# Kernel optimization log

Measured on AMD Instinct MI355X. Metric: run time of the kernel, lower is better.

The kernel has to match this reference:

```python
import jax, jax.numpy as jnp
import numpy as np
from collections import deque

N, IN_DIM, H, B, L = 512, 64, 128, 256, 2
SOURCE = 105
E_UND = 2048


def _build_graph_and_masks():
    rng = np.random.default_rng(0)
    s = rng.integers(0, N, E_UND)
    d = rng.integers(0, N, E_UND)
    edge_index = np.stack([np.concatenate([s, d]), np.concatenate([d, s])]).astype(np.int32)
    # BFS depths from source (undirected)
    adj = [[] for _ in range(N)]
    for a, b in zip(edge_index[0], edge_index[1]):
        adj[int(a)].append(int(b))
    depths = np.full(N, np.inf)
    depths[SOURCE] = 0.0
    q = deque([SOURCE]); seen = {SOURCE}
    while q:
        u = q.popleft()
        for v in adj[u]:
            if v not in seen:
                seen.add(v); depths[v] = depths[u] + 1.0; q.append(v)
    finite = np.isfinite(depths)
    maxd = depths[finite].max() if finite.any() else 0.0
    depths[~finite] = maxd + 1.0
    adj_mask = np.zeros((N, N), np.float32)
    adj_mask[edge_index[0], edge_index[1]] = 1.0
    adj_mask[edge_index[1], edge_index[0]] = 1.0
    np.fill_diagonal(adj_mask, 1.0)
    direction_mask = (depths[None, :] <= depths[:, None]).astype(np.float32)
    # admittance_matrix is None -> uniform init, then masked
    initial_causal = (np.ones((N, N), np.float32) / N) * adj_mask * direction_mask
    return edge_index, adj_mask, direction_mask, initial_causal


def setup_inputs() -> dict:
    key = jax.random.key(0)
    ks = jax.random.split(key, 16)
    edge_index, adj_mask, direction_mask, initial_causal = _build_graph_and_masks()
    w = lambda k, shp: jax.random.normal(k, shp, jnp.float32) * 0.02
    return {
        'x': jax.random.normal(ks[0], (B, N, IN_DIM), jnp.float32),
        'edge_index': jnp.asarray(edge_index),
        'adj_mask': jnp.asarray(adj_mask),
        'direction_mask': jnp.asarray(direction_mask),
        'causal_logits': jnp.asarray(initial_causal),  # nn.Parameter init
        'W_in': w(ks[1], (IN_DIM, H)), 'b_in': jnp.zeros((H,), jnp.float32),
        'Wq': w(ks[2], (H, H)), 'bq': jnp.zeros((H,), jnp.float32),
        'Wk': w(ks[3], (H, H)), 'bk': jnp.zeros((H,), jnp.float32),
        'Wv': w(ks[4], (H, H)), 'bv': jnp.zeros((H,), jnp.float32),
        'gcn_W': w(ks[5], (L, H, H)), 'gcn_b': jnp.zeros((L, H), jnp.float32),
        'W_fuse': w(ks[6], (2 * H, H)), 'b_fuse': jnp.zeros((H,), jnp.float32),
        'ln_g': jnp.ones((H,), jnp.float32), 'ln_b': jnp.zeros((H,), jnp.float32),
    }


def reference(x, edge_index, adj_mask, direction_mask, causal_logits,
              W_in, b_in, Wq, bq, Wk, bk, Wv, bv,
              gcn_W, gcn_b, W_fuse, b_fuse, ln_g, ln_b):
    n = adj_mask.shape[0]
    h = jax.nn.relu(x @ W_in + b_in)                               # (B,N,H)

    # causal matrix: softmax over learned logits, physically masked, renormalized
    C = jax.nn.softmax(causal_logits, axis=-1) * adj_mask * direction_mask
    C = C / jnp.clip(C.sum(-1, keepdims=True), 1e-8)

    # masked causal attention
    Q = h @ Wq + bq; K = h @ Wk + bk; V = h @ Wv + bv
    scale = jnp.asarray(h.shape[-1] ** 0.5, h.dtype)
    attn = jax.nn.softmax(jnp.einsum('bnh,bmh->bnm', Q, K) / scale, axis=-1)
    attn = attn * C[None]
    attn = attn / (attn.sum(-1, keepdims=True) + 1e-8)
    h_causal = jnp.einsum('bnm,bmh->bnh', attn, V)

    # GCNConv stack (self-loops + symmetric norm; dropout is identity in eval)
    src = jnp.concatenate([edge_index[0], jnp.arange(n, dtype=edge_index.dtype)])
    dst = jnp.concatenate([edge_index[1], jnp.arange(n, dtype=edge_index.dtype)])
    deg = jnp.zeros((n,), h.dtype).at[dst].add(1.0)
    dinv = deg ** -0.5                                              # deg>=1 (self loops)
    norm = (dinv[src] * dinv[dst])[None, :, None]                   # (1,E+N,1)
    h_g = h
    for l in range(gcn_W.shape[0]):
        hW = h_g @ gcn_W[l]                                         # (B,N,H)
        msg = hW[:, src, :] * norm                                  # (B,E+N,H)
        h_g = jnp.zeros_like(hW).at[:, dst, :].add(msg) + gcn_b[l]
        h_g = jax.nn.relu(h_g)

    h_comb = jnp.concatenate([h_causal, h_g], axis=-1) @ W_fuse + b_fuse
    mu = h_comb.mean(-1, keepdims=True)
    var = ((h_comb - mu) ** 2).mean(-1, keepdims=True)
    out = (h_comb - mu) / jnp.sqrt(var + 1e-5) * ln_g + ln_b
    return out, C
```

## Files before the change

### kernel.cpp

```cpp
#include <hip/hip_runtime.h>
#include <hip/hip_bf16.h>
#include <math.h>

#define NN 512
#define HH 128
#define INDIM 64
#define BB 256
#define NE 4096
#define MROWS (BB*NN)
#define OUT0 (BB*NN*HH)

typedef __attribute__((ext_vector_type(8))) short short8v;
typedef __attribute__((ext_vector_type(4))) float float4v;

__device__ __forceinline__ unsigned short f2bf(float f) {
  unsigned u = __float_as_uint(f);
  unsigned r = (u + 0x7fffu + ((u >> 16) & 1u)) >> 16;
  return (unsigned short)r;
}
__device__ __forceinline__ float bf2f(unsigned short b) {
  return __uint_as_float(((unsigned)b) << 16);
}

__global__ __launch_bounds__(256) void k_causalC(
    const float* __restrict__ logits, const float* __restrict__ adj,
    const float* __restrict__ dir, float* __restrict__ Cout)
{
  const int row = blockIdx.x;
  const int t = threadIdx.x;
  __shared__ float red[256];
  const float* lrow = logits + (size_t)row * NN;
  float v0 = lrow[t], v1 = lrow[t + 256];
  float mx = fmaxf(v0, v1);
  red[t] = mx; __syncthreads();
  for (int s = 128; s > 0; s >>= 1) { if (t < s) red[t] = fmaxf(red[t], red[t + s]); __syncthreads(); }
  mx = red[0]; __syncthreads();
  float e0 = __expf(v0 - mx), e1 = __expf(v1 - mx);
  red[t] = e0 + e1; __syncthreads();
  for (int s = 128; s > 0; s >>= 1) { if (t < s) red[t] += red[t + s]; __syncthreads(); }
  float sumE = red[0]; __syncthreads();
  float m0 = adj[(size_t)row * NN + t] * dir[(size_t)row * NN + t];
  float m1 = adj[(size_t)row * NN + t + 256] * dir[(size_t)row * NN + t + 256];
  float me0 = e0 * m0, me1 = e1 * m1;
  red[t] = me0 + me1; __syncthreads();
  for (int s = 128; s > 0; s >>= 1) { if (t < s) red[t] += red[t + s]; __syncthreads(); }
  float sumME = red[0];
  float sm = sumME / sumE;
  float denom = fmaxf(sm, 1e-8f) * sumE;
  Cout[(size_t)row * NN + t]       = me0 / denom;
  Cout[(size_t)row * NN + t + 256] = me1 / denom;
}

__global__ __launch_bounds__(512) void k_csr(const int* __restrict__ ei,
                                             int* __restrict__ rp,
                                             int* __restrict__ ci,
                                             float* __restrict__ cw)
{
  __shared__ int scnt[512];
  __shared__ float sdinv[512];
  __shared__ int sval[512];
  __shared__ int scur[512];
  const int t = threadIdx.x;
  const int* src = ei;
  const int* dst = ei + NE;
  scnt[t] = 0;
  __syncthreads();
  for (int e = t; e < NE; e += 512) atomicAdd(&scnt[dst[e]], 1);
  __syncthreads();
  const int deg = scnt[t] + 1;
  sdinv[t] = rsqrtf((float)deg);
  sval[t] = deg;
  __syncthreads();
  for (int off = 1; off < 512; off <<= 1) {
    int add = (t >= off) ? sval[t - off] : 0;
    __syncthreads();
    sval[t] += add;
    __syncthreads();
  }
  const int excl = sval[t] - deg;
  rp[t] = excl;
  if (t == 511) rp[512] = excl + deg;
  ci[excl] = t;
  cw[excl] = sdinv[t] * sdinv[t];
  scur[t] = excl + 1;
  __syncthreads();
  for (int e = t; e < NE; e += 512) {
    int s = src[e], d = dst[e];
    int p = atomicAdd(&scur[d], 1);
    ci[p] = s;
    cw[p] = sdinv[s] * sdinv[d];
  }
}

__global__ __launch_bounds__(512) void k_ccsr(const int* __restrict__ ei,
                                              const float* __restrict__ Cmat,
                                              int* __restrict__ rp,
                                              int* __restrict__ ci,
                                              float* __restrict__ cw)
{
  __shared__ unsigned bm[512 * 16];
  __shared__ int cnt[512];
  __shared__ int sval[512];
  __shared__ int cur[512];
  const int t = threadIdx.x;
  const int* src = ei;
  const int* dst = ei + NE;
  for (int i = t; i < 512 * 16; i += 512) bm[i] = 0u;
  __syncthreads();
  bm[t * 16 + (t >> 5)] |= (1u << (t & 31));
  cnt[t] = 1;
  __syncthreads();
  for (int e = t; e < NE; e += 512) {
    int r = src[e], c = dst[e];
    if (Cmat[(size_t)r * NN + c] > 0.f) {
      unsigned bit = 1u << (c & 31);
      unsigned old = atomicOr(&bm[r * 16 + (c >> 5)], bit);
      if (!(old & bit)) atomicAdd(&cnt[r], 1);
    }
  }
  __syncthreads();
  const int myc = cnt[t];
  sval[t] = myc;
  __syncthreads();
  for (int off = 1; off < 512; off <<= 1) {
    int add = (t >= off) ? sval[t - off] : 0;
    __syncthreads();
    sval[t] += add;
    __syncthreads();
  }
  const int excl = sval[t] - myc;
  rp[t] = excl;
  if (t == 511) rp[512] = excl + myc;
  ci[excl] = t;
  cw[excl] = Cmat[(size_t)t * NN + t];
  cur[t] = excl + 1;
  bm[t * 16 + (t >> 5)] &= ~(1u << (t & 31));
  __syncthreads();
  for (int e = t; e < NE; e += 512) {
    int r = src[e], c = dst[e];
    if (Cmat[(size_t)r * NN + c] > 0.f) {
      unsigned bit = 1u << (c & 31);
      unsigned old = atomicAnd(&bm[r * 16 + (c >> 5)], ~bit);
      if (old & bit) {
        int p = atomicAdd(&cur[r], 1);
        ci[p] = c;
        cw[p] = Cmat[(size_t)r * NN + c];
      }
    }
  }
}

__device__ __forceinline__ void gcn_body(
    int bid, const unsigned short* __restrict__ hW,
    const int* __restrict__ rp, const int* __restrict__ ci,
    const float* __restrict__ cw, const float* __restrict__ bias,
    unsigned short* __restrict__ out, int OS, int OC0)
{
  const int i5 = bid >> 3;
  const int ng = i5 & 31;
  const int b = (bid & 7) * 32 + (i5 >> 5);
  const int t = threadIdx.x;
  const int node = ng * 16 + (t >> 4);
  const int f0 = (t & 15) * 8;

  float bcol[8];
  #pragma unroll
  for (int k = 0; k < 8; k++) bcol[k] = bias[f0 + k];

  const unsigned short* base = hW + (size_t)b * 512 * 128;
  const int beg = rp[node], end = rp[node + 1];
  float acc[8] = {0.f, 0.f, 0.f, 0.f, 0.f, 0.f, 0.f, 0.f};
  for (int j = beg; j < end; j++) {
    int s = ci[j];
    float w = cw[j];
    short8v v = *(const short8v*)&base[(size_t)s * 128 + f0];
    #pragma unroll
    for (int k = 0; k < 8; k++) acc[k] += w * bf2f((unsigned short)v[k]);
  }
  short8v o;
  #pragma unroll
  for (int k = 0; k < 8; k++) {
    float v = fmaxf(acc[k] + bcol[k], 0.f);
    o[k] = (short)f2bf(v);
  }
  *(short8v*)&out[((size_t)(b * 512 + node)) * OS + OC0 + f0] = o;
}

__global__ __launch_bounds__(256) void k_gcn(
    const unsigned short* __restrict__ hW,
    const int* __restrict__ rp, const int* __restrict__ ci,
    const float* __restrict__ cw, const float* __restrict__ bias,
    unsigned short* __restrict__ out, int OS, int OC0)
{
  gcn_body(blockIdx.x, hW, rp, ci, cw, bias, out, OS, OC0);
}

__device__ __forceinline__ void sattn_body(
    int bid, const unsigned short* __restrict__ Qbf,
    const unsigned short* __restrict__ Kbf, const unsigned short* __restrict__ Vbf,
    const int* __restrict__ rp, const int* __restrict__ ci,
    const float* __restrict__ cw, unsigned short* __restrict__ Ocb)
{
  const int i5 = bid >> 3;
  const int ng = i5 & 31;
  const int b = (bid & 7) * 32 + (i5 >> 5);
  const int t = threadIdx.x;
  const int node = ng * 16 + (t >> 4);
  const int f0 = (t & 15) * 8;
  const float scale = 0.088388347648318447f;

  const size_t rowq = ((size_t)(b * 512 + node)) * 128 + f0;
  short8v qv = *(const short8v*)&Qbf[rowq];
  float qf[8];
  #pragma unroll
  for (int k = 0; k < 8; k++) qf[k] = bf2f((unsigned short)qv[k]);

  const unsigned short* Kb = Kbf + (size_t)b * 512 * 128;
  const unsigned short* Vb = Vbf + (size_t)b * 512 * 128;
  const int beg = rp[node], end = rp[node + 1];
  float acc[8] = {0.f, 0.f, 0.f, 0.f, 0.f, 0.f, 0.f, 0.f};
  float sw = 0.f;
  int j = beg;
  float w0 = cw[j];
  int m = ci[j];
  short8v kv = *(const short8v*)&Kb[(size_t)m * 128 + f0];
  short8v vv = *(const short8v*)&Vb[(size_t)m * 128 + f0];
  for (; j < end; ) {
    const int jn = (j + 1 < end) ? j + 1 : j;
    const float w02 = cw[jn];
    const int m2 = ci[jn];
    short8v kv2 = *(const short8v*)&Kb[(size_t)m2 * 128 + f0];
    short8v vv2 = *(const short8v*)&Vb[(size_t)m2 * 128 + f0];
    float part = 0.f;
    #pragma unroll
    for (int k = 0; k < 8; k++) part += qf[k] * bf2f((unsigned short)kv[k]);
    part += __shfl_xor(part, 1);
    part += __shfl_xor(part, 2);
    part += __shfl_xor(part, 4);
    part += __shfl_xor(part, 8);
    float w = __expf(part * scale) * w0;
    sw += w;
    #pragma unroll
    for (int k = 0; k < 8; k++) acc[k] += w * bf2f((unsigned short)vv[k]);
    j++;
    w0 = w02; kv = kv2; vv = vv2;
  }
  float inv = 1.0f / sw;
  short8v o;
  #pragma unroll
  for (int k = 0; k < 8; k++) o[k] = (short)f2bf(acc[k] * inv);
  *(short8v*)&Ocb[((size_t)(b * 512 + node)) * 256 + f0] = o;
}

__global__ __launch_bounds__(256) void k_gs(
    const unsigned short* __restrict__ hW,
    const int* __restrict__ grp, const int* __restrict__ gci,
    const float* __restrict__ gcw, const float* __restrict__ gbias,
    const unsigned short* __restrict__ Qbf, const unsigned short* __restrict__ Kbf,
    const unsigned short* __restrict__ Vbf,
    const int* __restrict__ arp, const int* __restrict__ aci,
    const float* __restrict__ acw,
    unsigned short* __restrict__ Dout)
{
  if (blockIdx.x < 8192)
    gcn_body(blockIdx.x, hW, grp, gci, gcw, gbias, Dout, 256, 128);
  else
    sattn_body(blockIdx.x - 8192, Qbf, Kbf, Vbf, arp, aci, acw, Dout);
}

__global__ __launch_bounds__(256) void k_wt(
    const float* s0, const float* s1, const float* s2, const float* s3,
    const float* s4, const float* s5, const float* s6,
    unsigned short* d0, unsigned short* d1, unsigned short* d2, unsigned short* d3,
    unsigned short* d4, unsigned short* d5, unsigned short* d6)
{
  const float* srcs[7] = {s0, s1, s2, s3, s4, s5, s6};
  unsigned short* dsts[7] = {d0, d1, d2, d3, d4, d5, d6};
  const int Ks[7] = {64, 128, 128, 128, 128, 128, 256};
  const int j = blockIdx.x >> 3;
  const int nc = blockIdx.x & 7;
  const float* s = srcs[j];
  unsigned short* d = dsts[j];
  const int K = Ks[j];
  const int STRW = K + 8;
  const int n0 = nc * 16;
  __shared__ short tile[16 * 264];
  const int t = threadIdx.x;
  for (int i = t; i < K * 16; i += 256) {
    int k = i >> 4, nn = i & 15;
    tile[nn * STRW + k] = (short)f2bf(s[k * 128 + n0 + nn]);
  }
  __syncthreads();
  for (int i = t; i < K * 2; i += 256) {
    int nn = (i * 8) / K;
    int k  = (i * 8) % K;
    *(short8v*)&d[(size_t)(n0 + nn) * K + k] =
        *(const short8v*)&tile[nn * STRW + k];
  }
}

template<bool RELU>
__global__ __launch_bounds__(256) void k_wgemm(
    const unsigned short* __restrict__ Abf,
    const unsigned short* __restrict__ Wt,
    const float* __restrict__ bias,
    unsigned short* __restrict__ Out)
{
  constexpr int STR = 136;
  __shared__ short Ws[128 * STR];
  __shared__ short rep[4 * 2048];
  const int t = threadIdx.x;
  const int wave = t >> 6, lane = t & 63;
  const int l15 = lane & 15, quad = lane >> 4;
  short* rw = rep + wave * 2048;

  for (int i = t; i < 128 * 16; i += 256) {
    int n = i >> 4, seg = i & 15;
    *(short8v*)&Ws[n * STR + seg * 8] =
        *(const short8v*)&Wt[(size_t)n * 128 + seg * 8];
  }
  float bcol[8];
  #pragma unroll
  for (int nt = 0; nt < 8; nt++) bcol[nt] = bias ? bias[nt * 16 + l15] : 0.f;
  __syncthreads();

  const int nwaves = gridDim.x * 4;
  int tile = blockIdx.x * 4 + wave;
  short8v af[4], afn[4];
  if (tile < MROWS / 16) {
    #pragma unroll
    for (int dc = 0; dc < 4; dc++)
      af[dc] = *(const short8v*)&Abf[((size_t)(tile * 16 + l15)) * 128 + dc * 32 + quad * 8];
  }
  while (tile < MROWS / 16) {
    const int ntile = tile + nwaves;
    if (ntile < MROWS / 16) {
      #pragma unroll
      for (int dc = 0; dc < 4; dc++)
        afn[dc] = *(const short8v*)&Abf[((size_t)(ntile * 16 + l15)) * 128 + dc * 32 + quad * 8];
    }
    float4v acc[8];
    #pragma unroll
    for (int nt = 0; nt < 8; nt++) acc[nt] = (float4v){0.f, 0.f, 0.f, 0.f};
    #pragma unroll
    for (int k32 = 0; k32 < 4; k32++) {
      #pragma unroll
      for (int nt = 0; nt < 8; nt++) {
        short8v wf = *(const short8v*)&Ws[(nt * 16 + l15) * STR + k32 * 32 + quad * 8];
        acc[nt] = __builtin_amdgcn_mfma_f32_16x16x32_bf16(af[k32], wf, acc[nt], 0, 0, 0);
      }
    }
    #pragma unroll
    for (int nt = 0; nt < 8; nt++)
      #pragma unroll
      for (int r = 0; r < 4; r++) {
        float v = acc[nt][r] + bcol[nt];
        if (RELU) v = fmaxf(v, 0.f);
        rw[(quad * 4 + r) * 128 + nt * 16 + l15] = (short)f2bf(v);
      }
    asm volatile("s_waitcnt lgkmcnt(0)" ::: "memory");
    __builtin_amdgcn_sched_barrier(0);
    #pragma unroll
    for (int p = 0; p < 4; p++) {
      int row16 = (lane >> 4) + p * 4, seg = lane & 15;
      short8v vv = *(const short8v*)&rw[row16 * 128 + seg * 8];
      *(short8v*)&Out[((size_t)(tile * 16 + row16)) * 128 + seg * 8] = vv;
    }
    tile = ntile;
    #pragma unroll
    for (int dc = 0; dc < 4; dc++) af[dc] = afn[dc];
  }
}

#define GNT 4
template<int KD, bool RELU, bool BATCHW, int OMODE, bool AF32>
__global__ __launch_bounds__(256) void k_bgemm(
    const void* __restrict__ Ap, const unsigned short* __restrict__ Wt,
    const float* __restrict__ bias, void* __restrict__ Out, int OS,
    const float* __restrict__ lng, const float* __restrict__ lnb)
{
  constexpr int KCH = (KD < 128) ? KD : 128;
  constexpr int STR = KCH + 8;
  constexpr bool WONCE = (KD <= 128);
  constexpr int ASH = (64 * STR > 8192) ? 64 * STR : 8192;
  constexpr int TRIPS = KCH / 32;
  __shared__ short lds[ASH + 128 * STR];
  short* As = lds;
  short* Ws = lds + ASH;
  const unsigned short* Abf = (const unsigned short*)Ap;
  const float* Af = (const float*)Ap;
  const int t = threadIdx.x;
  const int wave = t >> 6, lane = t & 63;
  const int l15 = lane & 15, quad = lane >> 4;

  short8v ap[TRIPS];
  float4 fa[TRIPS], fb[TRIPS];

  auto LOADC = [&](int rb, int kc) {
    #pragma unroll
    for (int j = 0; j < TRIPS; j++) {
      int i = t + j * 256;
      int r = i / (KCH / 8), seg = i % (KCH / 8);
      if (AF32) {
        const float* sp = &Af[(size_t)(rb + r) * KD + kc + seg * 8];
        fa[j] = *(const float4*)sp;
        fb[j] = *(const float4*)(sp + 4);
      } else {
        int arow = BATCHW ? ((rb & 511) + r) : (rb + r);
        ap[j] = *(const short8v*)&Abf[(size_t)arow * KD + kc + seg * 8];
      }
    }
  };
  auto STOREC = [&]() {
    #pragma unroll
    for (int j = 0; j < TRIPS; j++) {
      int i = t + j * 256;
      int r = i / (KCH / 8), seg = i % (KCH / 8);
      if (AF32) {
        short8v pk;
        pk[0] = (short)f2bf(fa[j].x); pk[1] = (short)f2bf(fa[j].y);
        pk[2] = (short)f2bf(fa[j].z); pk[3] = (short)f2bf(fa[j].w);
        pk[4] = (short)f2bf(fb[j].x); pk[5] = (short)f2bf(fb[j].y);
        pk[6] = (short)f2bf(fb[j].z); pk[7] = (short)f2bf(fb[j].w);
        *(short8v*)&As[r * STR + seg * 8] = pk;
      } else {
        *(short8v*)&As[r * STR + seg * 8] = ap[j];
      }
    }
  };

  float bcol[8];
  #pragma unroll
  for (int nt = 0; nt < 8; nt++) bcol[nt] = bias ? bias[nt * 16 + l15] : 0.f;
  float gcol[8], bbcol[8];
  if (OMODE == 2) {
    #pragma unroll
    for (int nt = 0; nt < 8; nt++) { gcol[nt] = lng[nt * 16 + l15]; bbcol[nt] = lnb[nt * 16 + l15]; }
  }

  for (int g = blockIdx.x; g < (MROWS / 64) / GNT; g += gridDim.x) {
    if (WONCE) {
      const int b0 = (g * GNT * 64) >> 9;
      const unsigned short* Wb = BATCHW ? (Wt + (size_t)b0 * 128 * KD) : Wt;
      for (int i = t; i < 128 * (KCH / 8); i += 256) {
        int n = i / (KCH / 8), seg = i % (KCH / 8);
        *(short8v*)&Ws[n * STR + seg * 8] =
            *(const short8v*)&Wb[(size_t)n * KD + seg * 8];
      }
    }
    LOADC(g * GNT * 64, 0);
    for (int tt = 0; tt < GNT; tt++) {
      const int tile = g * GNT + tt;
      const int rowbase = tile * 64;
      const int b = rowbase >> 9;
      float4v acc[8];
      #pragma unroll
      for (int nt = 0; nt < 8; nt++) acc[nt] = (float4v){0.f, 0.f, 0.f, 0.f};

      for (int kc = 0; kc < KD; kc += KCH) {
        __syncthreads();
        STOREC();
        if (!WONCE) {
          const unsigned short* Wb = BATCHW ? (Wt + (size_t)b * 128 * KD) : Wt;
          for (int i = t; i < 128 * (KCH / 8); i += 256) {
            int n = i / (KCH / 8), seg = i % (KCH / 8);
            *(short8v*)&Ws[n * STR + seg * 8] =
                *(const short8v*)&Wb[(size_t)n * KD + kc + seg * 8];
          }
        }
        __syncthreads();
        {
          int nkc = kc + KCH, ntt = tt;
          if (nkc >= KD) { nkc = 0; ntt = tt + 1; }
          if (ntt < GNT) LOADC((g * GNT + ntt) * 64, nkc);
        }
        #pragma unroll
        for (int k32 = 0; k32 < KCH / 32; k32++) {
          short8v af = *(const short8v*)&As[(wave * 16 + l15) * STR + k32 * 32 + quad * 8];
          #pragma unroll
          for (int nt = 0; nt < 8; nt++) {
            short8v wf = *(const short8v*)&Ws[(nt * 16 + l15) * STR + k32 * 32 + quad * 8];
            acc[nt] = __builtin_amdgcn_mfma_f32_16x16x32_bf16(af, wf, acc[nt], 0, 0, 0);
          }
        }
      }

      __syncthreads();
      if (OMODE == 0) {
        short* rep = As + wave * 2048;
        #pragma unroll
        for (int nt = 0; nt < 8; nt++)
          #pragma unroll
          for (int r = 0; r < 4; r++) {
            float v = acc[nt][r] + bcol[nt];
            if (RELU) v = fmaxf(v, 0.f);
            rep[(quad * 4 + r) * 128 + nt * 16 + l15] = (short)f2bf(v);
          }
        __syncthreads();
        unsigned short* Ob = (unsigned short*)Out;
        #pragma unroll
        for (int p = 0; p < 4; p++) {
          int row16 = (lane >> 4) + p * 4, seg = lane & 15;
          short8v vv = *(const short8v*)&rep[row16 * 128 + seg * 8];
          *(short8v*)&Ob[(size_t)(rowbase + wave * 16 + row16) * OS + seg * 8] = vv;
        }
      } else if (OMODE == 1) {
        short* rep = As + wave * 2048;
        #pragma unroll
        for (int nt = 0; nt < 8; nt++)
          #pragma unroll
          for (int r = 0; r < 4; r++) {
            float v = acc[nt][r] + bcol[nt];
            if (RELU) v = fmaxf(v, 0.f);
            rep[(nt * 16 + l15) * 16 + quad * 4 + r] = (short)f2bf(v);
          }
        __syncthreads();
        unsigned short* Ob = (unsigned short*)Out;
        int node0 = (rowbase & 511) + wave * 16;
        #pragma unroll
        for (int p = 0; p < 4; p++) {
          int idx = p * 64 + lane, c = idx >> 1, half = idx & 1;
          short8v vv = *(const short8v*)&rep[c * 16 + half * 8];
          *(short8v*)&Ob[((size_t)(b * 128 + c)) * 512 + node0 + half * 8] = vv;
        }
      } else {
        float* repw = (float*)lds + wave * 2048;
        float vv[8][4];
        float s[4] = {0, 0, 0, 0}, ss[4] = {0, 0, 0, 0};
        #pragma unroll
        for (int nt = 0; nt < 8; nt++)
          #pragma unroll
          for (int r = 0; r < 4; r++) {
            float v = acc[nt][r] + bcol[nt];
            vv[nt][r] = v;
            s[r] += v; ss[r] += v * v;
          }
        #pragma unroll
        for (int r = 0; r < 4; r++) {
          s[r] += __shfl_xor(s[r], 1);  s[r] += __shfl_xor(s[r], 2);
          s[r] += __shfl_xor(s[r], 4);  s[r] += __shfl_xor(s[r], 8);
          ss[r] += __shfl_xor(ss[r], 1); ss[r] += __shfl_xor(ss[r], 2);
          ss[r] += __shfl_xor(ss[r], 4); ss[r] += __shfl_xor(ss[r], 8);
        }
        #pragma unroll
        for (int r = 0; r < 4; r++) {
          float mu = s[r] * (1.0f / 128.0f);
          float var = ss[r] * (1.0f / 128.0f) - mu * mu;
          float inv = rsqrtf(var + 1e-5f);
          #pragma unroll
          for (int nt = 0; nt < 8; nt++)
            repw[(quad * 4 + r) * 128 + nt * 16 + l15] =
                (vv[nt][r] - mu) * inv * gcol[nt] + bbcol[nt];
        }
        __syncthreads();
        float* Of = (float*)Out;
        #pragma unroll
        for (int p = 0; p < 8; p++) {
          int row16 = (lane >> 5) + p * 2, seg = lane & 31;
          float4 o = *(const float4*)&repw[row16 * 128 + seg * 4];
          *(float4*)&Of[(size_t)(rowbase + wave * 16 + row16) * 128 + seg * 4] = o;
        }
      }
    }
  }
}

__global__ __launch_bounds__(256) void k_qkv4(
    const unsigned short* __restrict__ Abf,
    const unsigned short* __restrict__ W0, const unsigned short* __restrict__ W1,
    const unsigned short* __restrict__ W2, const unsigned short* __restrict__ W3,
    const float* __restrict__ b1, const float* __restrict__ b2,
    const float* __restrict__ b3,
    unsigned short* __restrict__ O0, unsigned short* __restrict__ O1,
    unsigned short* __restrict__ O2, unsigned short* __restrict__ O3)
{
  constexpr int STR = 136;
  __shared__ short lds[8704 + 128 * STR];
  short* As = lds;
  short* Ws = lds + 8704;
  const int t = threadIdx.x;
  const int wave = t >> 6, lane = t & 63;
  const int l15 = lane & 15, quad = lane >> 4;

  const unsigned short* Wsrc[4] = {W0, W1, W2, W3};
  const float* Bsrc[4] = {nullptr, b1, b2, b3};
  unsigned short* Osrc[4] = {O0, O1, O2, O3};

  short8v ap[4];
  auto LOADC = [&](int rb) {
    #pragma unroll
    for (int j = 0; j < 4; j++) {
      int i = t + j * 256;
      int r = i >> 4, seg = i & 15;
      ap[j] = *(const short8v*)&Abf[(size_t)(rb + r) * 128 + seg * 8];
    }
  };

  for (int g = blockIdx.x; g < (MROWS / 64) / GNT; g += gridDim.x) {
    #pragma unroll
    for (int s = 0; s < 4; s++) {
      for (int i = t; i < 128 * 16; i += 256) {
        int n = i >> 4, seg = i & 15;
        *(short8v*)&Ws[n * STR + seg * 8] =
            *(const short8v*)&Wsrc[s][(size_t)n * 128 + seg * 8];
      }
      float bcol[8];
      #pragma unroll
      for (int nt = 0; nt < 8; nt++) bcol[nt] = Bsrc[s] ? Bsrc[s][nt * 16 + l15] : 0.f;
      if (s == 0) LOADC(g * GNT * 64);

      for (int tt = 0; tt < GNT; tt++) {
        const int rowbase = (g * GNT + tt) * 64;
        float4v acc[8];
        #pragma unroll
        for (int nt = 0; nt < 8; nt++) acc[nt] = (float4v){0.f, 0.f, 0.f, 0.f};

        __syncthreads();
        #pragma unroll
        for (int j = 0; j < 4; j++) {
          int i = t + j * 256;
          int r = i >> 4, seg = i & 15;
          *(short8v*)&As[r * STR + seg * 8] = ap[j];
        }
        __syncthreads();

        {
          int ntt = tt + 1;
          if (ntt < GNT) LOADC((g * GNT + ntt) * 64);
          else if (s < 3) LOADC(g * GNT * 64);
        }

        #pragma unroll
        for (int k32 = 0; k32 < 4; k32++) {
          short8v af = *(const short8v*)&As[(wave * 16 + l15) * STR + k32 * 32 + quad * 8];
          #pragma unroll
          for (int nt = 0; nt < 8; nt++) {
            short8v wf = *(const short8v*)&Ws[(nt * 16 + l15) * STR + k32 * 32 + quad * 8];
            acc[nt] = __builtin_amdgcn_mfma_f32_16x16x32_bf16(af, wf, acc[nt], 0, 0, 0);
          }
        }
        __syncthreads();

        unsigned short* Ob = Osrc[s];
        short* rep = As + wave * 2048;
        #pragma unroll
        for (int nt = 0; nt < 8; nt++)
          #pragma unroll
          for (int r = 0; r < 4; r++) {
            float v = acc[nt][r] + bcol[nt];
            rep[(quad * 4 + r) * 128 + nt * 16 + l15] = (short)f2bf(v);
          }
        __syncthreads();
        #pragma unroll
        for (int p = 0; p < 4; p++) {
          int row16 = (lane >> 4) + p * 4, seg = lane & 15;
          short8v vv = *(const short8v*)&rep[row16 * 128 + seg * 8];
          *(short8v*)&Ob[(size_t)(rowbase + wave * 16 + row16) * 128 + seg * 8] = vv;
        }
      }
    }
  }
}

extern "C" void kernel_launch(void* const* d_in, const int* in_sizes, int n_in,
                              void* d_out, int out_size, void* d_ws, size_t ws_size,
                              hipStream_t stream)
{
  const float* x     = (const float*)d_in[0];
  const int*   ei    = (const int*)d_in[1];
  const float* adj   = (const float*)d_in[2];
  const float* dmask = (const float*)d_in[3];
  const float* clog  = (const float*)d_in[4];
  const float* W_in  = (const float*)d_in[5];
  const float* b_in  = (const float*)d_in[6];
  const float* Wq    = (const float*)d_in[7];
  const float* bq    = (const float*)d_in[8];
  const float* Wk    = (const float*)d_in[9];
  const float* bk    = (const float*)d_in[10];
  const float* Wv    = (const float*)d_in[11];
  const float* bv    = (const float*)d_in[12];
  const float* gcnW  = (const float*)d_in[13];
  const float* gcnB  = (const float*)d_in[14];
  const float* Wf    = (const float*)d_in[15];
  const float* bf    = (const float*)d_in[16];
  const float* lng   = (const float*)d_in[17];
  const float* lnb   = (const float*)d_in[18];

  float* outp = (float*)d_out;
  float* Cmat = outp + OUT0;

  char* W = (char*)d_ws;
  const size_t SLOT = (size_t)MROWS * 128 * 2;
  unsigned short* A0 = (unsigned short*)(W);
  unsigned short* B0 = (unsigned short*)(W + SLOT);
  unsigned short* C0 = (unsigned short*)(W + 2 * SLOT);
  unsigned short* D0 = (unsigned short*)(W + 3 * SLOT);
  char* AUX = W + 5 * SLOT;
  int*   csr_rp = (int*)AUX;
  int*   csr_ci = csr_rp + 640;
  float* csr_cw = (float*)(csr_ci + 4608);
  int*   crp    = (int*)(AUX + 131072);
  int*   cci    = crp + 640;
  float* ccw    = (float*)(cci + 8192);
  unsigned short* WB    = (unsigned short*)(AUX + 512 * 512 * 4) + 512 * 512 * 2;
  unsigned short* W_int = WB;
  unsigned short* Wqt   = WB + 8192;
  unsigned short* Wkt   = Wqt + 16384;
  unsigned short* Wvt   = Wkt + 16384;
  unsigned short* G0t   = Wvt + 16384;
  unsigned short* G1t   = G0t + 16384;
  unsigned short* Wft   = G1t + 16384;

  unsigned short* Vbf = (unsigned short*)outp;
  unsigned short* E0  = Vbf + (size_t)MROWS * 128;

  k_causalC<<<512, 256, 0, stream>>>(clog, adj, dmask, Cmat);
  k_csr<<<1, 512, 0, stream>>>(ei, csr_rp, csr_ci, csr_cw);
  k_ccsr<<<1, 512, 0, stream>>>(ei, Cmat, crp, cci, ccw);
  k_wt<<<56, 256, 0, stream>>>(W_in, Wq, Wk, Wv, gcnW, gcnW + HH * HH, Wf,
                               W_int, Wqt, Wkt, Wvt, G0t, G1t, Wft);

  k_bgemm<64, true, false, 0, true><<<512, 256, 0, stream>>>(
      x, W_int, b_in, B0, 128, nullptr, nullptr);
  k_qkv4<<<512, 256, 0, stream>>>(
      B0, G0t, Wqt, Wkt, Wvt, bq, bk, bv, A0, C0, E0, Vbf);
  k_gcn<<<8192, 256, 0, stream>>>(A0, csr_rp, csr_ci, csr_cw, gcnB, B0, 128, 0);
  k_wgemm<false><<<768, 256, 0, stream>>>(B0, G1t, nullptr, A0);
  k_gs<<<16384, 256, 0, stream>>>(
      A0, csr_rp, csr_ci, csr_cw, gcnB + HH,
      C0, E0, Vbf, crp, cci, ccw, D0);
  k_bgemm<256, false, false, 2, false><<<512, 256, 0, stream>>>(
      D0, Wft, bf, outp, 128, lng, lnb);
}
```

Measured before the change: 393.7 us.

## Fuse input projection into QKV/GCN projection kernel, keep activations in registers

Replaces the separate input-projection GEMM (x@W_in + bias + relu into B0) and the four-way projection kernel with one kernel. Each wave converts its x rows to bf16, computes the hidden tile with MFMA against W_in fragments held in registers, and keeps the resulting A fragments in registers across all four weight matrices. Per-wave LDS staging replaces block-wide A tiles, removing several __syncthreads and the global round trip of the hidden activation. The cost is higher register pressure (GNT×4 fragments plus W_in fragments) and reloading W_in fragments for every group.

```diff
diff --git a/kernel.cpp b/kernel.cpp
--- a/kernel.cpp
+++ b/kernel.cpp
@@ -565,8 +565,10 @@
   }
 }
 
-__global__ __launch_bounds__(256) void k_qkv4(
-    const unsigned short* __restrict__ Abf,
+__global__ __launch_bounds__(256) void k_hqkv4(
+    const float* __restrict__ x,
+    const unsigned short* __restrict__ Wint,
+    const float* __restrict__ bin,
     const unsigned short* __restrict__ W0, const unsigned short* __restrict__ W1,
     const unsigned short* __restrict__ W2, const unsigned short* __restrict__ W3,
     const float* __restrict__ b1, const float* __restrict__ b2,
@@ -575,30 +577,80 @@
     unsigned short* __restrict__ O2, unsigned short* __restrict__ O3)
 {
   constexpr int STR = 136;
-  __shared__ short lds[8704 + 128 * STR];
-  short* As = lds;
-  short* Ws = lds + 8704;
+  constexpr int RSTR = 136;
+  __shared__ short Ws[128 * STR];
+  __shared__ short rep[4 * 2304];
   const int t = threadIdx.x;
   const int wave = t >> 6, lane = t & 63;
   const int l15 = lane & 15, quad = lane >> 4;
+  short* rw = rep + wave * 2304;
 
   const unsigned short* Wsrc[4] = {W0, W1, W2, W3};
   const float* Bsrc[4] = {nullptr, b1, b2, b3};
   unsigned short* Osrc[4] = {O0, O1, O2, O3};
 
-  short8v ap[4];
-  auto LOADC = [&](int rb) {
-    #pragma unroll
-    for (int j = 0; j < 4; j++) {
-      int i = t + j * 256;
-      int r = i >> 4, seg = i & 15;
-      ap[j] = *(const short8v*)&Abf[(size_t)(rb + r) * 128 + seg * 8];
-    }
-  };
+  float bh[8];
+  #pragma unroll
+  for (int nt = 0; nt < 8; nt++) bh[nt] = bin[nt * 16 + l15];
 
   for (int g = blockIdx.x; g < (MROWS / 64) / GNT; g += gridDim.x) {
+    short8v wif[2][8];
+    #pragma unroll
+    for (int k32 = 0; k32 < 2; k32++)
+      #pragma unroll
+      for (int nt = 0; nt < 8; nt++)
+        wif[k32][nt] = *(const short8v*)&Wint[(size_t)(nt * 16 + l15) * 64 + k32 * 32 + quad * 8];
+
+    short8v af_all[GNT][4];
+    #pragma unroll
+    for (int tt = 0; tt < GNT; tt++) {
+      const int row0 = (g * GNT + tt) * 64 + wave * 16;
+      const float* xp = &x[(size_t)(row0 + l15) * 64 + quad * 16];
+      float4 fx0 = *(const float4*)(xp);
+      float4 fx1 = *(const float4*)(xp + 4);
+      float4 fx2 = *(const float4*)(xp + 8);
+      float4 fx3 = *(const float4*)(xp + 12);
+      short8v px0, px1;
+      px0[0] = (short)f2bf(fx0.x); px0[1] = (short)f2bf(fx0.y);
+      px0[2] = (short)f2bf(fx0.z); px0[3] = (short)f2bf(fx0.w);
+      px0[4] = (short)f2bf(fx1.x); px0[5] = (short)f2bf(fx1.y);
+      px0[6] = (short)f2bf(fx1.z); px0[7] = (short)f2bf(fx1.w);
+      px1[0] = (short)f2bf(fx2.x); px1[1] = (short)f2bf(fx2.y);
+      px1[2] = (short)f2bf(fx2.z); px1[3] = (short)f2bf(fx2.w);
+      px1[4] = (short)f2bf(fx3.x); px1[5] = (short)f2bf(fx3.y);
+      px1[6] = (short)f2bf(fx3.z); px1[7] = (short)f2bf(fx3.w);
+      *(short8v*)&rw[l15 * 72 + quad * 16]     = px0;
+      *(short8v*)&rw[l15 * 72 + quad * 16 + 8] = px1;
+      asm volatile("s_waitcnt lgkmcnt(0)" ::: "memory");
+      __builtin_amdgcn_sched_barrier(0);
+
+      float4v hacc[8];
+      #pragma unroll
+      for (int nt = 0; nt < 8; nt++) hacc[nt] = (float4v){0.f, 0.f, 0.f, 0.f};
+      #pragma unroll
+      for (int k32 = 0; k32 < 2; k32++) {
+        short8v ax = *(const short8v*)&rw[l15 * 72 + k32 * 32 + quad * 8];
+        #pragma unroll
+        for (int nt = 0; nt < 8; nt++)
+          hacc[nt] = __builtin_amdgcn_mfma_f32_16x16x32_bf16(ax, wif[k32][nt], hacc[nt], 0, 0, 0);
+      }
+      #pragma unroll
+      for (int nt = 0; nt < 8; nt++)
+        #pragma unroll
+        for (int r = 0; r < 4; r++) {
+          float v = fmaxf(hacc[nt][r] + bh[nt], 0.f);
+          rw[(quad * 4 + r) * RSTR + nt * 16 + l15] = (short)f2bf(v);
+        }
+      asm volatile("s_waitcnt lgkmcnt(0)" ::: "memory");
+      __builtin_amdgcn_sched_barrier(0);
+      #pragma unroll
+      for (int dc = 0; dc < 4; dc++)
+        af_all[tt][dc] = *(const short8v*)&rw[l15 * RSTR + dc * 32 + quad * 8];
+    }
+
     #pragma unroll
     for (int s = 0; s < 4; s++) {
+      __syncthreads();
       for (int i = t; i < 128 * 16; i += 256) {
         int n = i >> 4, seg = i & 15;
         *(short8v*)&Ws[n * STR + seg * 8] =
@@ -607,54 +659,36 @@
       float bcol[8];
       #pragma unroll
       for (int nt = 0; nt < 8; nt++) bcol[nt] = Bsrc[s] ? Bsrc[s][nt * 16 + l15] : 0.f;
-      if (s == 0) LOADC(g * GNT * 64);
-
+      __syncthreads();
+
+      #pragma unroll
       for (int tt = 0; tt < GNT; tt++) {
         const int rowbase = (g * GNT + tt) * 64;
         float4v acc[8];
         #pragma unroll
         for (int nt = 0; nt < 8; nt++) acc[nt] = (float4v){0.f, 0.f, 0.f, 0.f};
-
-        __syncthreads();
-        #pragma unroll
-        for (int j = 0; j < 4; j++) {
-          int i = t + j * 256;
-          int r = i >> 4, seg = i & 15;
-          *(short8v*)&As[r * STR + seg * 8] = ap[j];
-        }
-        __syncthreads();
-
-        {
-          int ntt = tt + 1;
-          if (ntt < GNT) LOADC((g * GNT + ntt) * 64);
-          else if (s < 3) LOADC(g * GNT * 64);
-        }
-
         #pragma unroll
         for (int k32 = 0; k32 < 4; k32++) {
-          short8v af = *(const short8v*)&As[(wave * 16 + l15) * STR + k32 * 32 + quad * 8];
           #pragma unroll
           for (int nt = 0; nt < 8; nt++) {
             short8v wf = *(const short8v*)&Ws[(nt * 16 + l15) * STR + k32 * 32 + quad * 8];
-            acc[nt] = __builtin_amdgcn_mfma_f32_16x16x32_bf16(af, wf, acc[nt], 0, 0, 0);
+            acc[nt] = __builtin_amdgcn_mfma_f32_16x16x32_bf16(af_all[tt][k32], wf, acc[nt], 0, 0, 0);
           }
         }
-        __syncthreads();
-
-        unsigned short* Ob = Osrc[s];
-        short* rep = As + wave * 2048;
         #pragma unroll
         for (int nt = 0; nt < 8; nt++)
           #pragma unroll
           for (int r = 0; r < 4; r++) {
             float v = acc[nt][r] + bcol[nt];
-            rep[(quad * 4 + r) * 128 + nt * 16 + l15] = (short)f2bf(v);
+            rw[(quad * 4 + r) * RSTR + nt * 16 + l15] = (short)f2bf(v);
           }
-        __syncthreads();
+        asm volatile("s_waitcnt lgkmcnt(0)" ::: "memory");
+        __builtin_amdgcn_sched_barrier(0);
+        unsigned short* Ob = Osrc[s];
         #pragma unroll
         for (int p = 0; p < 4; p++) {
           int row16 = (lane >> 4) + p * 4, seg = lane & 15;
-          short8v vv = *(const short8v*)&rep[row16 * 128 + seg * 8];
+          short8v vv = *(const short8v*)&rw[row16 * RSTR + seg * 8];
           *(short8v*)&Ob[(size_t)(rowbase + wave * 16 + row16) * 128 + seg * 8] = vv;
         }
       }
@@ -720,10 +754,8 @@
   k_wt<<<56, 256, 0, stream>>>(W_in, Wq, Wk, Wv, gcnW, gcnW + HH * HH, Wf,
                                W_int, Wqt, Wkt, Wvt, G0t, G1t, Wft);
 
-  k_bgemm<64, true, false, 0, true><<<512, 256, 0, stream>>>(
-      x, W_int, b_in, B0, 128, nullptr, nullptr);
-  k_qkv4<<<512, 256, 0, stream>>>(
-      B0, G0t, Wqt, Wkt, Wvt, bq, bk, bv, A0, C0, E0, Vbf);
+  k_hqkv4<<<512, 256, 0, stream>>>(
+      x, W_int, b_in, G0t, Wqt, Wkt, Wvt, bq, bk, bv, A0, C0, E0, Vbf);
   k_gcn<<<8192, 256, 0, stream>>>(A0, csr_rp, csr_ci, csr_cw, gcnB, B0, 128, 0);
   k_wgemm<false><<<768, 256, 0, stream>>>(B0, G1t, nullptr, A0);
   k_gs<<<16384, 256, 0, stream>>>(
```

Measured after the change: 392.8 us. No clear change (-0.2%).
